# Performance work log

Measured on AMD Instinct MI355X. Metric: run time of the kernel, lower is better.

## Reference

```python
import jax, jax.numpy as jnp
import numpy as np

# FNO 2D spectral conv: rfft2 -> keep 2 corner mode blocks -> complex einsum -> scatter -> irfft2
B, H, W, CIN, COUT = 8, 256, 256, 32, 32
M1, M2 = 16, 16
SCALE = 1.0 / (CIN * COUT)  # matches self.scale = 1/(in_channels*out_channels)


def setup_inputs() -> dict:
    key = jax.random.key(0)
    k1, k2, k3 = jax.random.split(key, 3)
    x = jax.random.normal(k1, (B, H, W, CIN), dtype=jnp.float32)  # channels_last input
    wshape = (2, CIN, COUT, M1, M2)  # (2**(ndims-1), in_c, out_c, m1, m2)
    w_real = (jax.random.uniform(k2, wshape, dtype=jnp.float32) * 2.0 - 1.0) * SCALE
    w_imag = (jax.random.uniform(k3, wshape, dtype=jnp.float32) * 2.0 - 1.0) * SCALE
    return {"x": x, "w_real": w_real, "w_imag": w_imag}


def reference(x, w_real, w_imag):
    w = jax.lax.complex(w_real, w_imag)  # complex64 spectral weights
    # channels_last -> channels_first: [B,H,W,C] -> [B,C,H,W]
    xc = jnp.transpose(x, (0, 3, 1, 2))
    x_ft = jnp.fft.rfft2(xc)  # [B, C, H, W//2+1] complex64
    # Two corner blocks along dim H (low and high freqs), low freqs along rfft dim.
    blocks = jnp.stack(
        [x_ft[:, :, :M1, :M2], x_ft[:, :, H - M1:, :M2]], axis=0
    )  # [2, B, Cin, M1, M2]
    # einsum 'wbi...,wio...->w...bo' (reordered here to wbohk; scatter layout equivalent)
    ob = jnp.einsum('wbihk,wiohk->wbohk', blocks, w)  # [2, B, Cout, M1, M2]
    out_ft = jnp.zeros((B, COUT, H, W // 2 + 1), dtype=ob.dtype)
    out_ft = out_ft.at[:, :, :M1, :M2].set(ob[0])
    out_ft = out_ft.at[:, :, H - M1:, :M2].set(ob[1])
    out = jnp.fft.irfft2(out_ft, s=(H, W))  # [B, Cout, H, W] float32
    # back to channels_last; activation is None (identity)
    return jnp.transpose(out, (0, 2, 3, 1))
```

## Files before the change

### kernel.cpp

```cpp
#include <hip/hip_runtime.h>
#include <math.h>


#define INV_HW (1.0f / 65536.0f)
#define STEP256 (6.28318530717958647692f / 256.0f)

__global__ __launch_bounds__(512) void k_wdft(const float* __restrict__ x,
                                              float* __restrict__ T) {
  __shared__ __align__(16) float sxe[2][32 * 136];
  __shared__ __align__(16) float sxo[2][32 * 136];
  __shared__ __align__(16) float4 sE[512];
  int t = threadIdx.x;
  int b = blockIdx.x >> 7, h0 = (blockIdx.x & 127) << 1;
  int sub = t >> 8, tsub = t & 255;
  const float4* src =
      (const float4*)(x + ((size_t)(b * 256 + h0 + sub)) * 8192);
  float4 av[4], bv[4];
#pragma unroll
  for (int i = 0; i < 4; ++i) {
    av[i] = src[tsub + 256 * i];
    bv[i] = src[tsub + 256 * i + 1024];
  }
  {
    int w = t >> 3, kwp = t & 7;
    int me = (2 * kwp * w) & 255, mo = ((2 * kwp + 1) * w) & 255;
    float se, ce, so, co;
    sincosf(STEP256 * (float)me, &se, &ce);
    sincosf(STEP256 * (float)mo, &so, &co);
    sE[t] = make_float4(ce, -se, co, -so);
  }
  float* pe = &sxe[sub][0];
  float* po = &sxo[sub][0];
#pragma unroll
  for (int i = 0; i < 4; ++i) {
    int j = tsub + 256 * i;
    int w = j >> 3, c0 = (j & 7) * 4;
    float4 a = av[i], bb = bv[i];
    pe[(c0 + 0) * 136 + w] = a.x + bb.x;
    pe[(c0 + 1) * 136 + w] = a.y + bb.y;
    pe[(c0 + 2) * 136 + w] = a.z + bb.z;
    pe[(c0 + 3) * 136 + w] = a.w + bb.w;
    po[(c0 + 0) * 136 + w] = a.x - bb.x;
    po[(c0 + 1) * 136 + w] = a.y - bb.y;
    po[(c0 + 2) * 136 + w] = a.z - bb.z;
    po[(c0 + 3) * 136 + w] = a.w - bb.w;
  }
  __syncthreads();
  int c = (t >> 3) & 31, kwp = t & 7;
  const float* xe = pe + c * 136;
  const float* xo = po + c * 136;
  const float4* eb = sE + kwp;
  float arl = 0, ail = 0, brl = 0, bil = 0;
  float arh = 0, aih = 0, brh = 0, bih = 0;
#pragma unroll 4
  for (int j = 0; j < 16; ++j) {
    float4 yel = *(const float4*)(xe + 4 * j);
    float4 yeh = *(const float4*)(xe + 64 + 4 * j);
    float4 yol = *(const float4*)(xo + 4 * j);
    float4 yoh = *(const float4*)(xo + 64 + 4 * j);
    float4 e0 = eb[(4 * j + 0) * 8];
    float4 e1 = eb[(4 * j + 1) * 8];
    float4 e2 = eb[(4 * j + 2) * 8];
    float4 e3 = eb[(4 * j + 3) * 8];
    arl += yel.x * e0.x; ail += yel.x * e0.y;
    brl += yol.x * e0.z; bil += yol.x * e0.w;
    arh += yeh.x * e0.x; aih += yeh.x * e0.y;
    brh += yoh.x * e0.z; bih += yoh.x * e0.w;
    arl += yel.y * e1.x; ail += yel.y * e1.y;
    brl += yol.y * e1.z; bil += yol.y * e1.w;
    arh += yeh.y * e1.x; aih += yeh.y * e1.y;
    brh += yoh.y * e1.z; bih += yoh.y * e1.w;
    arl += yel.z * e2.x; ail += yel.z * e2.y;
    brl += yol.z * e2.z; bil += yol.z * e2.w;
    arh += yeh.z * e2.x; aih += yeh.z * e2.y;
    brh += yoh.z * e2.z; bih += yoh.z * e2.w;
    arl += yel.w * e3.x; ail += yel.w * e3.y;
    brl += yol.w * e3.z; bil += yol.w * e3.w;
    arh += yeh.w * e3.x; aih += yeh.w * e3.y;
    brh += yoh.w * e3.z; bih += yoh.w * e3.w;
  }
  float sgn = (kwp & 1) ? -1.f : 1.f;
  float ar = fmaf(sgn, arh, arl);
  float ai = fmaf(sgn, aih, ail);
  float br = fmaf(sgn, bih, brl);
  float bi = fmaf(-sgn, brh, bil);
  int h = h0 + sub;
  ((float4*)(T + ((size_t)(b * 32 + c) * 256 + h) * 32))[kwp] =
      make_float4(ar, ai, br, bi);
}

__global__ __launch_bounds__(1024) void k_hdft(const float* __restrict__ T,
                                               float* __restrict__ X) {
  __shared__ __align__(16) float sT[8192];
  __shared__ float2 sU[256];
  __shared__ float4 sRed[768];
  int t = threadIdx.x;
  const float4* src = (const float4*)(T + (size_t)blockIdx.x * 8192);
  float4* dT = (float4*)sT;
  dT[t] = src[t];
  dT[t + 1024] = src[t + 1024];
  if (t < 256) {
    float s, c;
    sincosf(STEP256 * (float)t, &s, &c);
    sU[t] = make_float2(c, s);
  }
  __syncthreads();
  int kw = t & 15, kh = (t >> 4) & 15, s = t >> 8;
  float sg = (kh & 1) ? -1.f : 1.f;
  int st1 = kh, st2 = (kh + 240) & 255;
  int h0 = s * 32;
  int ph1 = (st1 * h0) & 255;
  int ph2 = (st2 * h0) & 255;
  float x0r = 0, x0i = 0, x1r = 0, x1i = 0;
#pragma unroll 4
  for (int hh = 0; hh < 32; ++hh) {
    int h = h0 + hh;
    float2 t0 = *(const float2*)(sT + h * 32 + kw * 2);
    float2 t1 = *(const float2*)(sT + (h + 128) * 32 + kw * 2);
    float tpx = fmaf(sg, t1.x, t0.x);
    float tpy = fmaf(sg, t1.y, t0.y);
    float2 e1 = sU[ph1];
    float2 e2 = sU[ph2];
    x0r += tpx * e1.x + tpy * e1.y;
    x0i += tpy * e1.x - tpx * e1.y;
    x1r += tpx * e2.x + tpy * e2.y;
    x1i += tpy * e2.x - tpx * e2.y;
    ph1 = (ph1 + st1) & 255;
    ph2 = (ph2 + st2) & 255;
  }
  if (s > 0) sRed[(s - 1) * 256 + (t & 255)] = make_float4(x0r, x0i, x1r, x1i);
  __syncthreads();
  if (s == 0) {
#pragma unroll
    for (int k = 0; k < 3; ++k) {
      float4 p = sRed[k * 256 + t];
      x0r += p.x; x0i += p.y; x1r += p.z; x1i += p.w;
    }
    float2* Xb = (float2*)(X + (size_t)blockIdx.x * 1024);
    Xb[kh * 16 + kw] = make_float2(x0r, x0i);
    Xb[(kh + 16) * 16 + kw] = make_float2(x1r, x1i);
  }
}

__global__ __launch_bounds__(512) void k_mixidft(const float* __restrict__ X,
                                                 const float* __restrict__ wr,
                                                 const float* __restrict__ wi,
                                                 float* __restrict__ G) {
  __shared__ __align__(16) float2 sY[512];
  __shared__ float2 sU[256];
  int b = blockIdx.x >> 5, o = blockIdx.x & 31;
  int t = threadIdx.x;
  if (t < 256) {
    float s, c;
    sincosf(STEP256 * (float)t, &s, &c);
    sU[t] = make_float2(c, s);
  }
  {
    int kw = t & 15, row = t >> 4;
    int blk = row >> 4, khl = row & 15;
    const float* wr0 =
        wr + (size_t)blk * 262144 + (size_t)o * 256 + khl * 16 + kw;
    const float* wi0 =
        wi + (size_t)blk * 262144 + (size_t)o * 256 + khl * 16 + kw;
    const float* Xb = X + (size_t)b * 32768 + row * 32 + kw * 2;
    float yr = 0, yi = 0;
#pragma unroll 4
    for (int i = 0; i < 32; ++i) {
      float2 xv = *(const float2*)(Xb + i * 1024);
      float a = wr0[i * 8192], bb = wi0[i * 8192];
      yr += xv.x * a - xv.y * bb;
      yi += xv.x * bb + xv.y * a;
    }
    sY[row * 16 + kw] = make_float2(yr, yi);
  }
  __syncthreads();
  const float4* sY4 = (const float4*)sY;
  int q = t & 7, hr = t >> 3;
#pragma unroll
  for (int hb = 0; hb < 2; ++hb) {
    int h = hr + hb * 64;
    float se0r = 0, se0i = 0, se1r = 0, se1i = 0;
    float so0r = 0, so0i = 0, so1r = 0, so1i = 0;
#pragma unroll 4
    for (int kh2 = 0; kh2 < 16; ++kh2) {
      int khe = 2 * kh2, kho = khe + 1;
      int khae = khe < 16 ? khe : khe + 224;
      int khao = kho < 16 ? kho : kho + 224;
      float2 ee = sU[(khae * h) & 255];
      float2 eo = sU[(khao * h) & 255];
      float4 yE = sY4[khe * 8 + q];
      float4 yO = sY4[kho * 8 + q];
      se0r += yE.x * ee.x - yE.y * ee.y;
      se0i += yE.x * ee.y + yE.y * ee.x;
      se1r += yE.z * ee.x - yE.w * ee.y;
      se1i += yE.z * ee.y + yE.w * ee.x;
      so0r += yO.x * eo.x - yO.y * eo.y;
      so0i += yO.x * eo.y + yO.y * eo.x;
      so1r += yO.z * eo.x - yO.w * eo.y;
      so1i += yO.z * eo.y + yO.w * eo.x;
    }
    float* g0 = G + (((size_t)b * 256 + h) * 32 + o) * 32 + 4 * q;
    float* g1 = G + (((size_t)b * 256 + h + 128) * 32 + o) * 32 + 4 * q;
    *(float4*)g0 =
        make_float4(se0r + so0r, se0i + so0i, se1r + so1r, se1i + so1i);
    *(float4*)g1 =
        make_float4(se0r - so0r, se0i - so0i, se1r - so1r, se1i - so1i);
  }
}

__global__ __launch_bounds__(256) void k_widft(const float* __restrict__ G,
                                               float* __restrict__ out) {
  __shared__ float sG[32 * 33];
  __shared__ __align__(16) float4 sE4[1024];
  int bh = blockIdx.x, t = threadIdx.x;
  float4 v = ((const float4*)(G + (size_t)bh * 1024))[t];
#pragma unroll
  for (int r = 0; r < 4; ++r) {
    int i = t + 256 * r;
    int w = i >> 3, q = i & 7;
    int me = (2 * q * w) & 255, mo = ((2 * q + 1) * w) & 255;
    float se, ce, so, co;
    sincosf(STEP256 * (float)me, &se, &ce);
    sincosf(STEP256 * (float)mo, &so, &co);
    float sc_e = (q == 0) ? INV_HW : 2.0f * INV_HW;
    sE4[i] = make_float4(sc_e * ce, sc_e * se, 2.0f * INV_HW * co,
                         2.0f * INV_HW * so);
  }
  {
    int o = t >> 3, p = t & 7;
    float* d = sG + o * 33 + p * 4;
    d[0] = v.x; d[1] = v.y; d[2] = v.z; d[3] = v.w;
  }
  __syncthreads();
  int o = t & 31, wb = t >> 5;
  float g[32];
#pragma unroll
  for (int k = 0; k < 32; ++k) g[k] = sG[o * 33 + k];
  float* ob = out + (size_t)bh * 8192 + o;
#pragma unroll 2
  for (int j = 0; j < 16; ++j) {
    int w = wb * 16 + j;
    float se = 0.f, so = 0.f;
#pragma unroll
    for (int q = 0; q < 8; ++q) {
      float4 e = sE4[w * 8 + q];
      se += g[4 * q] * e.x - g[4 * q + 1] * e.y;
      so += g[4 * q + 2] * e.z - g[4 * q + 3] * e.w;
    }
    ob[(size_t)w * 32] = se + so;
    ob[(size_t)(w + 128) * 32] = se - so;
  }
}

extern "C" void kernel_launch(void* const* d_in, const int* in_sizes, int n_in,
                              void* d_out, int out_size, void* d_ws,
                              size_t ws_size, hipStream_t stream) {
  const float* x = (const float*)d_in[0];
  const float* wr = (const float*)d_in[1];
  const float* wi = (const float*)d_in[2];
  float* out = (float*)d_out;
  float* ws = (float*)d_ws;

  float* T = ws;
  float* X = ws + 2097152;
  float* G = T;

  k_wdft<<<1024, 512, 0, stream>>>(x, T);
  k_hdft<<<256, 1024, 0, stream>>>(T, X);
  k_mixidft<<<256, 512, 0, stream>>>(X, wr, wi, G);
  k_widft<<<2048, 256, 0, stream>>>(G, out);
}
```

Before: 156.2 us.

## Split W-DFT input staging into two halves to halve LDS and overlap loads

The width-DFT kernel now stages the input row in two halves of 64 columns instead of all 128 at once, which halves its shared-memory footprint. The second half's global loads are issued right after the first sync, so they are in flight while the first half's DFT accumulation runs. This aims to raise occupancy and hide global-load latency. The cost is an extra pair of barriers and a second round of LDS stores per block.

```diff
diff --git a/kernel.cpp b/kernel.cpp
--- a/kernel.cpp
+++ b/kernel.cpp
@@ -7,17 +7,17 @@
 
 __global__ __launch_bounds__(512) void k_wdft(const float* __restrict__ x,
                                               float* __restrict__ T) {
-  __shared__ __align__(16) float sxe[2][32 * 136];
-  __shared__ __align__(16) float sxo[2][32 * 136];
+  __shared__ __align__(16) float sxe[2][32 * 68];
+  __shared__ __align__(16) float sxo[2][32 * 68];
   __shared__ __align__(16) float4 sE[512];
   int t = threadIdx.x;
   int b = blockIdx.x >> 7, h0 = (blockIdx.x & 127) << 1;
   int sub = t >> 8, tsub = t & 255;
   const float4* src =
       (const float4*)(x + ((size_t)(b * 256 + h0 + sub)) * 8192);
-  float4 av[4], bv[4];
-#pragma unroll
-  for (int i = 0; i < 4; ++i) {
+  float4 av[2], bv[2];
+#pragma unroll
+  for (int i = 0; i < 2; ++i) {
     av[i] = src[tsub + 256 * i];
     bv[i] = src[tsub + 256 * i + 1024];
   }
@@ -32,52 +32,80 @@
   float* pe = &sxe[sub][0];
   float* po = &sxo[sub][0];
 #pragma unroll
-  for (int i = 0; i < 4; ++i) {
+  for (int i = 0; i < 2; ++i) {
     int j = tsub + 256 * i;
     int w = j >> 3, c0 = (j & 7) * 4;
     float4 a = av[i], bb = bv[i];
-    pe[(c0 + 0) * 136 + w] = a.x + bb.x;
-    pe[(c0 + 1) * 136 + w] = a.y + bb.y;
-    pe[(c0 + 2) * 136 + w] = a.z + bb.z;
-    pe[(c0 + 3) * 136 + w] = a.w + bb.w;
-    po[(c0 + 0) * 136 + w] = a.x - bb.x;
-    po[(c0 + 1) * 136 + w] = a.y - bb.y;
-    po[(c0 + 2) * 136 + w] = a.z - bb.z;
-    po[(c0 + 3) * 136 + w] = a.w - bb.w;
-  }
-  __syncthreads();
+    pe[(c0 + 0) * 68 + w] = a.x + bb.x;
+    pe[(c0 + 1) * 68 + w] = a.y + bb.y;
+    pe[(c0 + 2) * 68 + w] = a.z + bb.z;
+    pe[(c0 + 3) * 68 + w] = a.w + bb.w;
+    po[(c0 + 0) * 68 + w] = a.x - bb.x;
+    po[(c0 + 1) * 68 + w] = a.y - bb.y;
+    po[(c0 + 2) * 68 + w] = a.z - bb.z;
+    po[(c0 + 3) * 68 + w] = a.w - bb.w;
+  }
+  __syncthreads();
+#pragma unroll
+  for (int i = 0; i < 2; ++i) {
+    av[i] = src[tsub + 256 * i + 512];
+    bv[i] = src[tsub + 256 * i + 1536];
+  }
   int c = (t >> 3) & 31, kwp = t & 7;
-  const float* xe = pe + c * 136;
-  const float* xo = po + c * 136;
+  const float* xe = pe + c * 68;
+  const float* xo = po + c * 68;
   const float4* eb = sE + kwp;
   float arl = 0, ail = 0, brl = 0, bil = 0;
   float arh = 0, aih = 0, brh = 0, bih = 0;
 #pragma unroll 4
   for (int j = 0; j < 16; ++j) {
-    float4 yel = *(const float4*)(xe + 4 * j);
-    float4 yeh = *(const float4*)(xe + 64 + 4 * j);
-    float4 yol = *(const float4*)(xo + 4 * j);
-    float4 yoh = *(const float4*)(xo + 64 + 4 * j);
+    float4 ye = *(const float4*)(xe + 4 * j);
+    float4 yo = *(const float4*)(xo + 4 * j);
     float4 e0 = eb[(4 * j + 0) * 8];
     float4 e1 = eb[(4 * j + 1) * 8];
     float4 e2 = eb[(4 * j + 2) * 8];
     float4 e3 = eb[(4 * j + 3) * 8];
-    arl += yel.x * e0.x; ail += yel.x * e0.y;
-    brl += yol.x * e0.z; bil += yol.x * e0.w;
-    arh += yeh.x * e0.x; aih += yeh.x * e0.y;
-    brh += yoh.x * e0.z; bih += yoh.x * e0.w;
-    arl += yel.y * e1.x; ail += yel.y * e1.y;
-    brl += yol.y * e1.z; bil += yol.y * e1.w;
-    arh += yeh.y * e1.x; aih += yeh.y * e1.y;
-    brh += yoh.y * e1.z; bih += yoh.y * e1.w;
-    arl += yel.z * e2.x; ail += yel.z * e2.y;
-    brl += yol.z * e2.z; bil += yol.z * e2.w;
-    arh += yeh.z * e2.x; aih += yeh.z * e2.y;
-    brh += yoh.z * e2.z; bih += yoh.z * e2.w;
-    arl += yel.w * e3.x; ail += yel.w * e3.y;
-    brl += yol.w * e3.z; bil += yol.w * e3.w;
-    arh += yeh.w * e3.x; aih += yeh.w * e3.y;
-    brh += yoh.w * e3.z; bih += yoh.w * e3.w;
+    arl += ye.x * e0.x; ail += ye.x * e0.y;
+    brl += yo.x * e0.z; bil += yo.x * e0.w;
+    arl += ye.y * e1.x; ail += ye.y * e1.y;
+    brl += yo.y * e1.z; bil += yo.y * e1.w;
+    arl += ye.z * e2.x; ail += ye.z * e2.y;
+    brl += yo.z * e2.z; bil += yo.z * e2.w;
+    arl += ye.w * e3.x; ail += ye.w * e3.y;
+    brl += yo.w * e3.z; bil += yo.w * e3.w;
+  }
+  __syncthreads();
+#pragma unroll
+  for (int i = 0; i < 2; ++i) {
+    int j = tsub + 256 * i;
+    int w = j >> 3, c0 = (j & 7) * 4;
+    float4 a = av[i], bb = bv[i];
+    pe[(c0 + 0) * 68 + w] = a.x + bb.x;
+    pe[(c0 + 1) * 68 + w] = a.y + bb.y;
+    pe[(c0 + 2) * 68 + w] = a.z + bb.z;
+    pe[(c0 + 3) * 68 + w] = a.w + bb.w;
+    po[(c0 + 0) * 68 + w] = a.x - bb.x;
+    po[(c0 + 1) * 68 + w] = a.y - bb.y;
+    po[(c0 + 2) * 68 + w] = a.z - bb.z;
+    po[(c0 + 3) * 68 + w] = a.w - bb.w;
+  }
+  __syncthreads();
+#pragma unroll 4
+  for (int j = 0; j < 16; ++j) {
+    float4 ye = *(const float4*)(xe + 4 * j);
+    float4 yo = *(const float4*)(xo + 4 * j);
+    float4 e0 = eb[(4 * j + 0) * 8];
+    float4 e1 = eb[(4 * j + 1) * 8];
+    float4 e2 = eb[(4 * j + 2) * 8];
+    float4 e3 = eb[(4 * j + 3) * 8];
+    arh += ye.x * e0.x; aih += ye.x * e0.y;
+    brh += yo.x * e0.z; bih += yo.x * e0.w;
+    arh += ye.y * e1.x; aih += ye.y * e1.y;
+    brh += yo.y * e1.z; bih += yo.y * e1.w;
+    arh += ye.z * e2.x; aih += ye.z * e2.y;
+    brh += yo.z * e2.z; bih += yo.z * e2.w;
+    arh += ye.w * e3.x; aih += ye.w * e3.y;
+    brh += yo.w * e3.z; bih += yo.w * e3.w;
   }
   float sgn = (kwp & 1) ? -1.f : 1.f;
   float ar = fmaf(sgn, arh, arl);
```

New measurement: 157.6 us. About the same (+0.9%).
